# Performance work log

Hardware: AMD Instinct MI355X
Metric: run time of the kernel (lower is better)

The kernel has to match this reference:

```python
import jax, jax.numpy as jnp
import numpy as np

D = 128          # fine voxel grid resolution
N0 = 250000
D_IN, D_BASE, D_OUT = 16, 8, 8
EPS = 1e-5
# (cin, cout) for conv0..conv6, conv7, conv9, conv11
_CH = [(16, 8), (8, 16), (16, 16), (16, 32), (32, 32), (32, 64), (64, 64), (64, 32), (32, 16), (16, 8)]

def _offsets():
    r = np.arange(-1, 2)
    return np.stack(np.meshgrid(r, r, r, indexing='ij'), -1).reshape(-1, 3)  # [27,3]

def _lookup_fn(coords, d):
    keys = (coords[:, 0].astype(np.int64) * d + coords[:, 1]) * d + coords[:, 2]
    order = np.argsort(keys)
    skeys = keys[order]
    def lookup(q):
        valid = ((q >= 0) & (q < d)).all(-1)
        k = (q[:, 0].astype(np.int64) * d + q[:, 1]) * d + q[:, 2]
        pos = np.clip(np.searchsorted(skeys, k), 0, len(skeys) - 1)
        return np.where(valid & (skeys[pos] == k), order[pos], -1).astype(np.int32)
    return lookup

def _nbr_same(coords, d):
    # stride-1 sparse conv: outputs at input coords, neighbors at coord+k
    lk = _lookup_fn(coords, d)
    return np.stack([lk(coords + o) for o in _offsets()], 1)  # [N,27]

def _nbr_down(c_out, c_in, d_in):
    # stride-2 conv: output p gathers inputs at 2p+k
    lk = _lookup_fn(c_in, d_in)
    return np.stack([lk(c_out * 2 + o) for o in _offsets()], 1)

def _nbr_up(c_out, c_in, d_in):
    # transposed stride-2 conv: output q gathers input p=(q-k)/2 where divisible
    lk = _lookup_fn(c_in, d_in)
    cols = []
    for o in _offsets():
        q = c_out - o
        div = (q % 2 == 0).all(-1)
        cols.append(np.where(div, lk(q // 2), -1).astype(np.int32))
    return np.stack(cols, 1)

def setup_inputs():
    rng = np.random.default_rng(0)
    flat = rng.choice(D ** 3, size=N0, replace=False)
    c0 = np.stack([flat // (D * D), (flat // D) % D, flat % D], 1).astype(np.int32)
    c1 = np.unique(c0 // 2, axis=0)
    c2 = np.unique(c1 // 2, axis=0)
    c3 = np.unique(c2 // 2, axis=0)
    inp = {
        'feats': jax.random.normal(jax.random.key(0), (N0, D_IN), jnp.float32),
        'nbr0': jnp.asarray(_nbr_same(c0, D)),
        'nbr_d01': jnp.asarray(_nbr_down(c1, c0, D)),
        'nbr1': jnp.asarray(_nbr_same(c1, D // 2)),
        'nbr_d12': jnp.asarray(_nbr_down(c2, c1, D // 2)),
        'nbr2': jnp.asarray(_nbr_same(c2, D // 4)),
        'nbr_d23': jnp.asarray(_nbr_down(c3, c2, D // 4)),
        'nbr3': jnp.asarray(_nbr_same(c3, D // 8)),
        'nbr_u32': jnp.asarray(_nbr_up(c2, c3, D // 8)),
        'nbr_u21': jnp.asarray(_nbr_up(c1, c2, D // 4)),
        'nbr_u10': jnp.asarray(_nbr_up(c0, c1, D // 2)),
    }
    key = jax.random.key(1)
    for i, (ci, co) in enumerate(_CH):
        key, kw = jax.random.split(key)
        inp['w%d' % i] = jax.random.normal(kw, (27, ci, co), jnp.float32) / np.sqrt(27.0 * ci)
        inp['g%d' % i] = jnp.ones((co,), jnp.float32)
        inp['b%d' % i] = jnp.zeros((co,), jnp.float32)
    inp['lin_w'] = jax.random.normal(jax.random.key(2), (D_OUT, D_BASE), jnp.float32) / np.sqrt(D_BASE)
    return inp

def _sconv_bn_relu(f, nbr, w, g, b):
    # f: [Nin,Cin], nbr: [Nout,27] (-1 = no neighbor), w: [27,Cin,Cout]
    gth = jnp.where((nbr >= 0)[..., None], f[jnp.maximum(nbr, 0)], 0.0)  # [Nout,27,Cin]
    y = jnp.einsum('nkc,kco->no', gth, w)
    mu = y.mean(0)                       # training-mode BatchNorm over active voxels
    var = y.var(0)
    return jax.nn.relu((y - mu) * jax.lax.rsqrt(var + EPS) * g + b)

def reference(feats, nbr0, nbr_d01, nbr1, nbr_d12, nbr2, nbr_d23, nbr3, nbr_u32, nbr_u21, nbr_u10,
              w0, g0, b0, w1, g1, b1, w2, g2, b2, w3, g3, b3, w4, g4, b4,
              w5, g5, b5, w6, g6, b6, w7, g7, b7, w8, g8, b8, w9, g9, b9, lin_w):
    c0f = _sconv_bn_relu(feats, nbr0, w0, g0, b0)
    c2f = _sconv_bn_relu(_sconv_bn_relu(c0f, nbr_d01, w1, g1, b1), nbr1, w2, g2, b2)
    c4f = _sconv_bn_relu(_sconv_bn_relu(c2f, nbr_d12, w3, g3, b3), nbr2, w4, g4, b4)
    x = _sconv_bn_relu(_sconv_bn_relu(c4f, nbr_d23, w5, g5, b5), nbr3, w6, g6, b6)
    x = c4f + _sconv_bn_relu(x, nbr_u32, w7, g7, b7)
    x = c2f + _sconv_bn_relu(x, nbr_u21, w8, g8, b8)
    x = c0f + _sconv_bn_relu(x, nbr_u10, w9, g9, b9)
    return x @ lin_w.T, x
```

## Files before the change

### kernel.cpp

```cpp
#include <hip/hip_runtime.h>

#define EPSV 1e-5f

typedef __attribute__((ext_vector_type(8))) short short8;
typedef __attribute__((ext_vector_type(4))) float float4v;

static inline int cdiv(int a, int b) { return (a + b - 1) / b; }

__device__ inline unsigned short f2bf(float x) {
  unsigned u = __float_as_uint(x);
  return (unsigned short)((u + 0x7FFFu + ((u >> 16) & 1u)) >> 16);
}
__device__ inline float bf2f(unsigned short u) {
  return __uint_as_float(((unsigned)u) << 16);
}

#define NBUCKET 16

struct PrepArgs {
  const float* w[10];
  unsigned short* wt[10];
  int ci[10];
  int co[10];
  int wcum[11];
  const float* feats;
  unsigned short* featsb;
  int nfeat4;
  float* stats;
};

__global__ __launch_bounds__(256) void prep_kernel(PrepArgs p) {
  long tid = (long)blockIdx.x * 256 + threadIdx.x;
  const int nstat4 = 10 * NBUCKET * 128 / 4;
  if (tid < nstat4) {
    ((float4*)p.stats)[tid] = make_float4(0.f, 0.f, 0.f, 0.f);
    return;
  }
  tid -= nstat4;
  if (tid < p.nfeat4) {
    float4 v = ((const float4*)p.feats)[tid];
    ushort4 r;
    r.x = f2bf(v.x); r.y = f2bf(v.y); r.z = f2bf(v.z); r.w = f2bf(v.w);
    ((ushort4*)p.featsb)[tid] = r;
    return;
  }
  tid -= p.nfeat4;
  if (tid >= p.wcum[10]) return;
  int i = 0;
  while (tid >= p.wcum[i + 1]) ++i;
  int e = (int)(tid - p.wcum[i]);
  int ci = p.ci[i], co = p.co[i];
  int k = e / (ci * co);
  int r = e - k * (ci * co);
  int o = r / ci;
  int c = r - o * ci;
  p.wt[i][((long)k * co + o) * ci + c] = f2bf(p.w[i][((long)k * ci + c) * co + o]);
}

template<int CI, int CO>
__global__ __launch_bounds__(256) void conv_mfma(
    const unsigned short* __restrict__ f, const int* __restrict__ nbr,
    const unsigned short* __restrict__ wt, float* __restrict__ y,
    float* __restrict__ stats, int nout, int nxb) {
  constexpr int NCHUNK = (CI == 8) ? 7 : (CI == 16) ? 14 : (CI == 32) ? 27 : 54;

  int bx = blockIdx.x, xb;
  {
    int S8 = nxb >> 3;
    if (bx < (S8 << 3)) xb = (bx & 7) * S8 + (bx >> 3);
    else xb = bx;
  }

  const int tid = threadIdx.x;
  const int lane = tid & 63;
  const int wid = tid >> 6;
  const int m = lane & 15;
  const int quad = lane >> 4;
  const int blockrow = xb * 64;
  const int row = blockrow + wid * 16 + m;
  const bool rok = row < nout;
  const int cbase = blockIdx.y * 16;
  const int co = cbase + m;
  const bool cok = co < CO;

  auto tapof = [&](int c) -> int {
    if constexpr (CI == 8) return c * 4 + quad;
    else if constexpr (CI == 16) return c * 2 + (quad >> 1);
    else if constexpr (CI == 32) return c;
    else return c >> 1;
  };
  auto cioof = [&](int c) -> int {
    if constexpr (CI == 8) return 0;
    else if constexpr (CI == 16) return (quad & 1) * 8;
    else if constexpr (CI == 32) return quad * 8;
    else return ((c & 1) << 5) + quad * 8;
  };

  float4v acc = {0.f, 0.f, 0.f, 0.f};

  if constexpr (CI <= 16) {
    int idxs[NCHUNK];
#pragma unroll
    for (int c = 0; c < NCHUNK; ++c) {
      int tap = tapof(c);
      idxs[c] = (rok && tap < 27) ? nbr[(long)row * 27 + tap] : -1;
    }
    short8 A[NCHUNK], B[NCHUNK];
#pragma unroll
    for (int c = 0; c < NCHUNK; ++c) {
      int tap = tapof(c);
      short8 a, bq;
#pragma unroll
      for (int q = 0; q < 8; ++q) { a[q] = 0; bq[q] = 0; }
      if (idxs[c] >= 0) a = *(const short8*)(f + (long)idxs[c] * CI + cioof(c));
      if (cok && tap < 27) bq = *(const short8*)(wt + ((long)tap * CO + co) * CI + cioof(c));
      A[c] = a; B[c] = bq;
    }
#pragma unroll
    for (int c = 0; c < NCHUNK; ++c)
      acc = __builtin_amdgcn_mfma_f32_16x16x32_bf16(A[c], B[c], acc, 0, 0, 0);
  } else {
    constexpr int G = 9;
    constexpr int NG = NCHUNK / G;
    int idxs[27];
#pragma unroll
    for (int t = 0; t < 27; ++t)
      idxs[t] = rok ? nbr[(long)row * 27 + t] : -1;

    short8 A[2][G], B[2][G];
    auto load_group = [&](int g, int bi) {
#pragma unroll
      for (int j = 0; j < G; ++j) {
        const int c = g * G + j;
        const int tap = tapof(c);
        short8 a, bq;
#pragma unroll
        for (int q = 0; q < 8; ++q) { a[q] = 0; bq[q] = 0; }
        int idx = idxs[tap];
        if (idx >= 0) a = *(const short8*)(f + (long)idx * CI + cioof(c));
        if (cok) bq = *(const short8*)(wt + ((long)tap * CO + co) * CI + cioof(c));
        A[bi][j] = a; B[bi][j] = bq;
      }
    };
    load_group(0, 0);
#pragma unroll
    for (int g = 0; g < NG; ++g) {
      const int cur = g & 1;
      if (g + 1 < NG) load_group(g + 1, cur ^ 1);
#pragma unroll
      for (int j = 0; j < G; ++j)
        acc = __builtin_amdgcn_mfma_f32_16x16x32_bf16(A[cur][j], B[cur][j], acc, 0, 0, 0);
    }
  }

  float sum = 0.f, sq = 0.f;
#pragma unroll
  for (int r = 0; r < 4; ++r) {
    float v = acc[r];
    int orow = blockrow + wid * 16 + quad * 4 + r;
    if (cok && orow < nout) y[(long)orow * CO + co] = v;
    sum += v;
    sq = fmaf(v, v, sq);
  }
  sum += __shfl_xor(sum, 16); sq += __shfl_xor(sq, 16);
  sum += __shfl_xor(sum, 32); sq += __shfl_xor(sq, 32);
  if (quad == 0 && cok) {
    float* st = stats + (((unsigned)xb & (NBUCKET - 1)) << 7);
    atomicAdd(&st[co], sum);
    atomicAdd(&st[64 + co], sq);
  }
}

template<int CO>
__global__ __launch_bounds__(256) void bn_relu_bf16(
    const float* __restrict__ y, const float* __restrict__ stats,
    const float* __restrict__ g, const float* __restrict__ b,
    const unsigned short* __restrict__ skip, unsigned short* __restrict__ out,
    int nout, float inv_n) {
  __shared__ float sA[CO], sC[CO];
  if ((int)threadIdx.x < CO) {
    int o = threadIdx.x;
    float su = 0.f, sq = 0.f;
#pragma unroll
    for (int bk = 0; bk < NBUCKET; ++bk) {
      su += stats[bk * 128 + o];
      sq += stats[bk * 128 + 64 + o];
    }
    float mu = su * inv_n;
    float var = sq * inv_n - mu * mu;
    float a = g[o] * rsqrtf(var + EPSV);
    sA[o] = a;
    sC[o] = fmaf(-mu, a, b[o]);
  }
  __syncthreads();
  long i4 = (long)blockIdx.x * 256 + threadIdx.x;
  long total4 = (long)nout * CO / 4;
  if (i4 >= total4) return;
  int o = (int)((i4 * 4) % CO);
  float4 v = ((const float4*)y)[i4];
  float vv[4] = {v.x, v.y, v.z, v.w};
  unsigned short rr[4];
#pragma unroll
  for (int j = 0; j < 4; ++j) {
    float x = fmaxf(fmaf(vv[j], sA[o + j], sC[o + j]), 0.f);
    if (skip) x += bf2f(skip[i4 * 4 + j]);
    rr[j] = f2bf(x);
  }
  ushort4 r;
  r.x = rr[0]; r.y = rr[1]; r.z = rr[2]; r.w = rr[3];
  ((ushort4*)out)[i4] = r;
}

__global__ __launch_bounds__(256) void tail_kernel(
    const unsigned short* __restrict__ c0f, const float* __restrict__ st9,
    const float* __restrict__ g9, const float* __restrict__ b9, float inv_n,
    const float* __restrict__ lin_w, float* y9out, float* __restrict__ x0, int n0) {
  __shared__ float swl[64];
  __shared__ float sbn[16];
  if (threadIdx.x < 64) swl[threadIdx.x] = lin_w[threadIdx.x];
  if (threadIdx.x < 8) {
    int o = threadIdx.x;
    float su = 0.f, sq = 0.f;
#pragma unroll
    for (int bk = 0; bk < NBUCKET; ++bk) {
      su += st9[bk * 128 + o];
      sq += st9[bk * 128 + 64 + o];
    }
    float mu = su * inv_n;
    float var = sq * inv_n - mu * mu;
    float a = g9[o] * rsqrtf(var + EPSV);
    sbn[o] = a;
    sbn[8 + o] = fmaf(-mu, a, b9[o]);
  }
  __syncthreads();
  int n = blockIdx.x * 256 + threadIdx.x;
  if (n >= n0) return;
  const float4* pr = (const float4*)(y9out + (long)n * 8);
  float4 r0 = pr[0], r1 = pr[1];
  float rr[8] = {r0.x, r0.y, r0.z, r0.w, r1.x, r1.y, r1.z, r1.w};
  const ushort4* pc = (const ushort4*)(c0f + (long)n * 8);
  ushort4 c0 = pc[0], c1 = pc[1];
  unsigned short cs[8] = {c0.x, c0.y, c0.z, c0.w, c1.x, c1.y, c1.z, c1.w};
  float xv[8];
#pragma unroll
  for (int c = 0; c < 8; ++c)
    xv[c] = bf2f(cs[c]) + fmaxf(fmaf(rr[c], sbn[c], sbn[8 + c]), 0.f);
  *(float4*)(x0 + (long)n * 8) = make_float4(xv[0], xv[1], xv[2], xv[3]);
  *(float4*)(x0 + (long)n * 8 + 4) = make_float4(xv[4], xv[5], xv[6], xv[7]);
  float ov[8];
#pragma unroll
  for (int j = 0; j < 8; ++j) {
    float s = 0.f;
#pragma unroll
    for (int c = 0; c < 8; ++c) s = fmaf(xv[c], swl[j * 8 + c], s);
    ov[j] = s;
  }
  *(float4*)(y9out + (long)n * 8) = make_float4(ov[0], ov[1], ov[2], ov[3]);
  *(float4*)(y9out + (long)n * 8 + 4) = make_float4(ov[4], ov[5], ov[6], ov[7]);
}

extern "C" void kernel_launch(void* const* d_in, const int* in_sizes, int n_in,
                              void* d_out, int out_size, void* d_ws, size_t ws_size,
                              hipStream_t stream) {
  const float* feats   = (const float*)d_in[0];
  const int* nbr0      = (const int*)d_in[1];
  const int* nbr_d01   = (const int*)d_in[2];
  const int* nbr1      = (const int*)d_in[3];
  const int* nbr_d12   = (const int*)d_in[4];
  const int* nbr2      = (const int*)d_in[5];
  const int* nbr_d23   = (const int*)d_in[6];
  const int* nbr3      = (const int*)d_in[7];
  const int* nbr_u32   = (const int*)d_in[8];
  const int* nbr_u21   = (const int*)d_in[9];
  const int* nbr_u10   = (const int*)d_in[10];
  const float* w[10];
  const float* g[10];
  const float* b[10];
  for (int i = 0; i < 10; ++i) {
    w[i] = (const float*)d_in[11 + 3 * i];
    g[i] = (const float*)d_in[12 + 3 * i];
    b[i] = (const float*)d_in[13 + 3 * i];
  }
  const float* lin_w = (const float*)d_in[41];

  const int N0 = in_sizes[0] / 16;
  const int N1 = in_sizes[2] / 27;
  const int N2 = in_sizes[4] / 27;
  const int N3 = in_sizes[6] / 27;
  const float i0 = 1.f / N0, i1 = 1.f / N1, i2 = 1.f / N2, i3 = 1.f / N3;

  static const int CIv[10] = {16, 8, 16, 16, 32, 32, 64, 64, 32, 16};
  static const int COv[10] = {8, 16, 16, 32, 32, 64, 64, 32, 16, 8};

  float* stats = (float*)d_ws;
  float* yraw  = stats + 10 * NBUCKET * 128;
  unsigned short* u = (unsigned short*)(yraw + (size_t)N1 * 16);

  unsigned short* wt[10];
  int wcum[11];
  wcum[0] = 0;
  for (int i = 0; i < 10; ++i) {
    wt[i] = u;
    int sz = 27 * CIv[i] * COv[i];
    u += sz;
    wcum[i + 1] = wcum[i] + sz;
  }
  unsigned short* featsb = u; u += (size_t)N0 * 16;
  unsigned short* c0f = u;    u += (size_t)N0 * 8;
  unsigned short* t1  = u;    u += (size_t)N1 * 16;
  unsigned short* c2f = u;    u += (size_t)N1 * 16;
  unsigned short* t2  = u;    u += (size_t)N2 * 32;
  unsigned short* c4f = u;    u += (size_t)N2 * 32;
  unsigned short* t3  = u;    u += (size_t)N3 * 64;
  unsigned short* t4  = u;    u += (size_t)N3 * 64;
  unsigned short* t5  = t2;
  unsigned short* t6  = t1;
  float* y9 = (float*)d_out;
  float* x0 = (float*)d_out + (size_t)N0 * 8;

  float* s[10];
  for (int i = 0; i < 10; ++i) s[i] = stats + i * NBUCKET * 128;

  PrepArgs pa;
  for (int i = 0; i < 10; ++i) {
    pa.w[i] = w[i]; pa.wt[i] = wt[i];
    pa.ci[i] = CIv[i]; pa.co[i] = COv[i];
    pa.wcum[i] = wcum[i];
  }
  pa.wcum[10] = wcum[10];
  pa.feats = feats; pa.featsb = featsb;
  pa.nfeat4 = N0 * 16 / 4;
  pa.stats = stats;
  long prep_total = (10 * NBUCKET * 128 / 4) + pa.nfeat4 + wcum[10];
  prep_kernel<<<(int)((prep_total + 255) / 256), 256, 0, stream>>>(pa);

  auto bgrid = [](long nout, int co) { return (int)((nout * co / 4 + 255) / 256); };

  int xb0 = cdiv(N0, 64), xb1 = cdiv(N1, 64), xb2 = cdiv(N2, 64), xb3 = cdiv(N3, 64);

  conv_mfma<16, 8><<<dim3(xb0, 1), 256, 0, stream>>>(featsb, nbr0, wt[0], yraw, s[0], N0, xb0);
  bn_relu_bf16<8><<<bgrid(N0, 8), 256, 0, stream>>>(yraw, s[0], g[0], b[0], nullptr, c0f, N0, i0);

  conv_mfma<8, 16><<<dim3(xb1, 1), 256, 0, stream>>>(c0f, nbr_d01, wt[1], yraw, s[1], N1, xb1);
  bn_relu_bf16<16><<<bgrid(N1, 16), 256, 0, stream>>>(yraw, s[1], g[1], b[1], nullptr, t1, N1, i1);

  conv_mfma<16, 16><<<dim3(xb1, 1), 256, 0, stream>>>(t1, nbr1, wt[2], yraw, s[2], N1, xb1);
  bn_relu_bf16<16><<<bgrid(N1, 16), 256, 0, stream>>>(yraw, s[2], g[2], b[2], nullptr, c2f, N1, i1);

  conv_mfma<16, 32><<<dim3(xb2, 2), 256, 0, stream>>>(c2f, nbr_d12, wt[3], yraw, s[3], N2, xb2);
  bn_relu_bf16<32><<<bgrid(N2, 32), 256, 0, stream>>>(yraw, s[3], g[3], b[3], nullptr, t2, N2, i2);

  conv_mfma<32, 32><<<dim3(xb2, 2), 256, 0, stream>>>(t2, nbr2, wt[4], yraw, s[4], N2, xb2);
  bn_relu_bf16<32><<<bgrid(N2, 32), 256, 0, stream>>>(yraw, s[4], g[4], b[4], nullptr, c4f, N2, i2);

  conv_mfma<32, 64><<<dim3(xb3, 4), 256, 0, stream>>>(c4f, nbr_d23, wt[5], yraw, s[5], N3, xb3);
  bn_relu_bf16<64><<<bgrid(N3, 64), 256, 0, stream>>>(yraw, s[5], g[5], b[5], nullptr, t3, N3, i3);

  conv_mfma<64, 64><<<dim3(xb3, 4), 256, 0, stream>>>(t3, nbr3, wt[6], yraw, s[6], N3, xb3);
  bn_relu_bf16<64><<<bgrid(N3, 64), 256, 0, stream>>>(yraw, s[6], g[6], b[6], nullptr, t4, N3, i3);

  conv_mfma<64, 32><<<dim3(xb2, 2), 256, 0, stream>>>(t4, nbr_u32, wt[7], yraw, s[7], N2, xb2);
  bn_relu_bf16<32><<<bgrid(N2, 32), 256, 0, stream>>>(yraw, s[7], g[7], b[7], c4f, t5, N2, i2);

  conv_mfma<32, 16><<<dim3(xb1, 1), 256, 0, stream>>>(t5, nbr_u21, wt[8], yraw, s[8], N1, xb1);
  bn_relu_bf16<16><<<bgrid(N1, 16), 256, 0, stream>>>(yraw, s[8], g[8], b[8], c2f, t6, N1, i1);

  conv_mfma<16, 8><<<dim3(xb0, 1), 256, 0, stream>>>(t6, nbr_u10, wt[9], y9, s[9], N0, xb0);

  tail_kernel<<<cdiv(N0, 256), 256, 0, stream>>>(c0f, s[9], g[9], b[9], i0, lin_w, y9, x0, N0);
}
```

Before: 489.8 us.

## Store raw conv outputs as bf16 and widen BN stat buckets

The pre-BatchNorm conv outputs are now written to a bf16 scratch buffer instead of fp32, including the last-level conv output that previously went into the output buffer. This halves write and read traffic between each conv and its BN/ReLU kernel. The atomic statistics buckets grow from 16 to 64 to reduce atomic contention, at the cost of a longer per-channel reduction in the BN kernels. Statistics are still accumulated in fp32, but normalisation is applied to bf16-rounded values, which adds some precision error.

Result: slower. 501.8 us (+2.5%).

```diff
diff --git a/kernel.cpp b/kernel.cpp
--- a/kernel.cpp
+++ b/kernel.cpp
@@ -15,7 +15,7 @@
   return __uint_as_float(((unsigned)u) << 16);
 }
 
-#define NBUCKET 16
+#define NBUCKET 64
 
 struct PrepArgs {
   const float* w[10];
@@ -60,7 +60,7 @@
 template<int CI, int CO>
 __global__ __launch_bounds__(256) void conv_mfma(
     const unsigned short* __restrict__ f, const int* __restrict__ nbr,
-    const unsigned short* __restrict__ wt, float* __restrict__ y,
+    const unsigned short* __restrict__ wt, unsigned short* __restrict__ y,
     float* __restrict__ stats, int nout, int nxb) {
   constexpr int NCHUNK = (CI == 8) ? 7 : (CI == 16) ? 14 : (CI == 32) ? 27 : 54;
 
@@ -158,7 +158,7 @@
   for (int r = 0; r < 4; ++r) {
     float v = acc[r];
     int orow = blockrow + wid * 16 + quad * 4 + r;
-    if (cok && orow < nout) y[(long)orow * CO + co] = v;
+    if (cok && orow < nout) y[(long)orow * CO + co] = f2bf(v);
     sum += v;
     sq = fmaf(v, v, sq);
   }
@@ -173,7 +173,7 @@
 
 template<int CO>
 __global__ __launch_bounds__(256) void bn_relu_bf16(
-    const float* __restrict__ y, const float* __restrict__ stats,
+    const unsigned short* __restrict__ y, const float* __restrict__ stats,
     const float* __restrict__ g, const float* __restrict__ b,
     const unsigned short* __restrict__ skip, unsigned short* __restrict__ out,
     int nout, float inv_n) {
@@ -181,7 +181,7 @@
   if ((int)threadIdx.x < CO) {
     int o = threadIdx.x;
     float su = 0.f, sq = 0.f;
-#pragma unroll
+#pragma unroll 8
     for (int bk = 0; bk < NBUCKET; ++bk) {
       su += stats[bk * 128 + o];
       sq += stats[bk * 128 + 64 + o];
@@ -197,8 +197,8 @@
   long total4 = (long)nout * CO / 4;
   if (i4 >= total4) return;
   int o = (int)((i4 * 4) % CO);
-  float4 v = ((const float4*)y)[i4];
-  float vv[4] = {v.x, v.y, v.z, v.w};
+  ushort4 v = ((const ushort4*)y)[i4];
+  float vv[4] = {bf2f(v.x), bf2f(v.y), bf2f(v.z), bf2f(v.w)};
   unsigned short rr[4];
 #pragma unroll
   for (int j = 0; j < 4; ++j) {
@@ -214,14 +214,15 @@
 __global__ __launch_bounds__(256) void tail_kernel(
     const unsigned short* __restrict__ c0f, const float* __restrict__ st9,
     const float* __restrict__ g9, const float* __restrict__ b9, float inv_n,
-    const float* __restrict__ lin_w, float* y9out, float* __restrict__ x0, int n0) {
+    const float* __restrict__ lin_w, const unsigned short* __restrict__ y9,
+    float* __restrict__ out0, float* __restrict__ x0, int n0) {
   __shared__ float swl[64];
   __shared__ float sbn[16];
   if (threadIdx.x < 64) swl[threadIdx.x] = lin_w[threadIdx.x];
   if (threadIdx.x < 8) {
     int o = threadIdx.x;
     float su = 0.f, sq = 0.f;
-#pragma unroll
+#pragma unroll 8
     for (int bk = 0; bk < NBUCKET; ++bk) {
       su += st9[bk * 128 + o];
       sq += st9[bk * 128 + 64 + o];
@@ -235,16 +236,16 @@
   __syncthreads();
   int n = blockIdx.x * 256 + threadIdx.x;
   if (n >= n0) return;
-  const float4* pr = (const float4*)(y9out + (long)n * 8);
-  float4 r0 = pr[0], r1 = pr[1];
-  float rr[8] = {r0.x, r0.y, r0.z, r0.w, r1.x, r1.y, r1.z, r1.w};
+  const ushort4* pr = (const ushort4*)(y9 + (long)n * 8);
+  ushort4 r0 = pr[0], r1 = pr[1];
+  unsigned short rw[8] = {r0.x, r0.y, r0.z, r0.w, r1.x, r1.y, r1.z, r1.w};
   const ushort4* pc = (const ushort4*)(c0f + (long)n * 8);
   ushort4 c0 = pc[0], c1 = pc[1];
   unsigned short cs[8] = {c0.x, c0.y, c0.z, c0.w, c1.x, c1.y, c1.z, c1.w};
   float xv[8];
 #pragma unroll
   for (int c = 0; c < 8; ++c)
-    xv[c] = bf2f(cs[c]) + fmaxf(fmaf(rr[c], sbn[c], sbn[8 + c]), 0.f);
+    xv[c] = bf2f(cs[c]) + fmaxf(fmaf(bf2f(rw[c]), sbn[c], sbn[8 + c]), 0.f);
   *(float4*)(x0 + (long)n * 8) = make_float4(xv[0], xv[1], xv[2], xv[3]);
   *(float4*)(x0 + (long)n * 8 + 4) = make_float4(xv[4], xv[5], xv[6], xv[7]);
   float ov[8];
@@ -255,8 +256,8 @@
     for (int c = 0; c < 8; ++c) s = fmaf(xv[c], swl[j * 8 + c], s);
     ov[j] = s;
   }
-  *(float4*)(y9out + (long)n * 8) = make_float4(ov[0], ov[1], ov[2], ov[3]);
-  *(float4*)(y9out + (long)n * 8 + 4) = make_float4(ov[4], ov[5], ov[6], ov[7]);
+  *(float4*)(out0 + (long)n * 8) = make_float4(ov[0], ov[1], ov[2], ov[3]);
+  *(float4*)(out0 + (long)n * 8 + 4) = make_float4(ov[4], ov[5], ov[6], ov[7]);
 }
 
 extern "C" void kernel_launch(void* const* d_in, const int* in_sizes, int n_in,
@@ -293,8 +294,9 @@
   static const int COv[10] = {8, 16, 16, 32, 32, 64, 64, 32, 16, 8};
 
   float* stats = (float*)d_ws;
-  float* yraw  = stats + 10 * NBUCKET * 128;
-  unsigned short* u = (unsigned short*)(yraw + (size_t)N1 * 16);
+  unsigned short* u = (unsigned short*)(stats + 10 * NBUCKET * 128);
+
+  unsigned short* yraw = u; u += (size_t)N1 * 32;
 
   unsigned short* wt[10];
   int wcum[11];
@@ -315,8 +317,8 @@
   unsigned short* t4  = u;    u += (size_t)N3 * 64;
   unsigned short* t5  = t2;
   unsigned short* t6  = t1;
-  float* y9 = (float*)d_out;
-  float* x0 = (float*)d_out + (size_t)N0 * 8;
+  float* out0 = (float*)d_out;
+  float* x0   = (float*)d_out + (size_t)N0 * 8;
 
   float* s[10];
   for (int i = 0; i < 10; ++i) s[i] = stats + i * NBUCKET * 128;
@@ -365,7 +367,7 @@
   conv_mfma<32, 16><<<dim3(xb1, 1), 256, 0, stream>>>(t5, nbr_u21, wt[8], yraw, s[8], N1, xb1);
   bn_relu_bf16<16><<<bgrid(N1, 16), 256, 0, stream>>>(yraw, s[8], g[8], b[8], c2f, t6, N1, i1);
 
-  conv_mfma<16, 8><<<dim3(xb0, 1), 256, 0, stream>>>(t6, nbr_u10, wt[9], y9, s[9], N0, xb0);
-
-  tail_kernel<<<cdiv(N0, 256), 256, 0, stream>>>(c0f, s[9], g[9], b[9], i0, lin_w, y9, x0, N0);
-}
+  conv_mfma<16, 8><<<dim3(xb0, 1), 256, 0, stream>>>(t6, nbr_u10, wt[9], yraw, s[9], N0, xb0);
+
+  tail_kernel<<<cdiv(N0, 256), 256, 0, stream>>>(c0f, s[9], g[9], b[9], i0, lin_w, yraw, out0, x0, N0);
+}
```
